# Kernel optimization log

Measured on AMD Instinct MI355X. Metric: run time of the kernel, lower is better.

## Reference

```python
import jax, jax.numpy as jnp
import numpy as np

B, N, M, H, W = 8, 8192, 4096, 128, 128


def setup_inputs() -> dict:
    key = jax.random.key(0)
    k1, k2, k3, k4 = jax.random.split(key, 4)
    xc_off_grid = jax.random.uniform(k1, (B, N, 2), dtype=jnp.float32)
    yc_off_grid = jax.random.normal(k2, (B, N), dtype=jnp.float32)
    # regular grid coords: meshgrid of two sorted 1-D axes, stacked on last dim
    xs = jnp.linspace(0.0, 1.0, H, dtype=jnp.float32)
    ys = jnp.linspace(0.0, 1.0, W, dtype=jnp.float32)
    gx, gy = jnp.meshgrid(xs, ys, indexing='ij')  # [H,W]
    xc_on_grid = jnp.broadcast_to(jnp.stack([gx, gy], -1), (B, H, W, 2))
    yc_on_grid = jax.random.normal(k3, (B, H, W), dtype=jnp.float32)
    # targets slightly outside [0,1] so interpn fill_value path is exercised
    xt = jax.random.uniform(k4, (B, M, 2), minval=-0.05, maxval=1.05, dtype=jnp.float32)
    mix_prop_logit = jnp.asarray(0.0, dtype=jnp.float32)
    return {"xc_off_grid": xc_off_grid, "yc_off_grid": yc_off_grid,
            "xc_on_grid": xc_on_grid, "yc_on_grid": yc_on_grid,
            "xt": xt, "mix_prop_logit": mix_prop_logit}


def _bilinear(xs, ys, vals, pts, fill):
    # interpn((xs, ys), vals, pts, bounds_error=False, fill_value=fill)
    x, y = pts[:, 0], pts[:, 1]
    ix = jnp.clip(jnp.searchsorted(xs, x, side='right') - 1, 0, xs.shape[0] - 2)
    iy = jnp.clip(jnp.searchsorted(ys, y, side='right') - 1, 0, ys.shape[0] - 2)
    wx = (x - xs[ix]) / (xs[ix + 1] - xs[ix])
    wy = (y - ys[iy]) / (ys[iy + 1] - ys[iy])
    v00 = vals[ix, iy]
    v01 = vals[ix, iy + 1]
    v10 = vals[ix + 1, iy]
    v11 = vals[ix + 1, iy + 1]
    v = ((1 - wx) * (1 - wy) * v00 + (1 - wx) * wy * v01
         + wx * (1 - wy) * v10 + wx * wy * v11)
    oob = (x < xs[0]) | (x > xs[-1]) | (y < ys[0]) | (y > ys[-1])
    return jnp.where(oob, fill, v)


def _per_batch(xc_off, yc_off, xc_on, yc_on, pts):
    # scattered interpolation: nearest-neighbor gather (stands in for
    # scipy griddata's Delaunay-linear; same irregular-access pattern)
    d2 = jnp.sum((pts[:, None, :] - xc_off[None, :, :]) ** 2, axis=-1)  # [M,N]
    yt_off = yc_off[jnp.argmin(d2, axis=1)]  # [M]
    # regular-grid bilinear, fill with grid mean outside bounds
    yt_on = _bilinear(xc_on[:, 0, 0], xc_on[0, :, 1], yc_on, pts, yc_on.mean())
    return yt_off, yt_on


def reference(xc_off_grid, yc_off_grid, xc_on_grid, yc_on_grid, xt, mix_prop_logit):
    yt_off, yt_on = jax.vmap(_per_batch)(xc_off_grid, yc_off_grid,
                                         xc_on_grid, yc_on_grid, xt)
    mix = jax.nn.sigmoid(mix_prop_logit)
    return mix * yt_off + (1 - mix) * yt_on  # [B, M]
```

## Files before the change

### kernel.cpp

```cpp
#include <hip/hip_runtime.h>
#include <math.h>
#include <float.h>

#define BB 8
#define NN 8192
#define MM 4096
#define HH 128
#define WW 128

#define G    32
#define GG   (G * G)
#define CELL (1.0f / G)

#define WS_COUNTS_OFF 256
#define WS_STARTS_OFF 33024
#define WS_CELLS_OFF  65824
#define WS_NEEDED     (WS_CELLS_OFF + (size_t)BB * NN * 16)

__device__ __forceinline__ int clampi(int v, int lo, int hi) {
    return v < lo ? lo : (v > hi ? hi : v);
}

__global__ void mean_zero_kernel(const float* __restrict__ yc_on,
                                 float* __restrict__ means,
                                 int* __restrict__ counts) {
    int b = blockIdx.x;
    if (counts) {
        int* c = counts + b * GG;
        for (int i = threadIdx.x; i < GG; i += blockDim.x) c[i] = 0;
    }
    const float* p = yc_on + b * (HH * WW);
    float s = 0.f;
    for (int i = threadIdx.x; i < HH * WW; i += blockDim.x) s += p[i];
    for (int off = 32; off > 0; off >>= 1) s += __shfl_down(s, off, 64);
    __shared__ float partial[4];
    int wave = threadIdx.x >> 6;
    if ((threadIdx.x & 63) == 0) partial[wave] = s;
    __syncthreads();
    if (threadIdx.x == 0) {
        float t = 0.f;
        int nw = blockDim.x >> 6;
        for (int i = 0; i < nw; ++i) t += partial[i];
        means[b] = t * (1.0f / (HH * WW));
    }
}

__global__ __launch_bounds__(256)
void count_kernel(const float* __restrict__ xc_off,
                  int* __restrict__ counts) {
    const int i = blockIdx.x * blockDim.x + threadIdx.x;
#pragma unroll
    for (int k = 0; k < 2; ++k) {
        const int idx = i + k * 32768;
        const int b = idx >> 13;
        const float2 c = ((const float2*)xc_off)[idx];
        const int gx = clampi((int)(c.x * (float)G), 0, G - 1);
        const int gy = clampi((int)(c.y * (float)G), 0, G - 1);
        atomicAdd(&counts[b * GG + gx * G + gy], 1);
    }
}

__global__ __launch_bounds__(1024)
void scan_kernel(int* __restrict__ counts,
                 int* __restrict__ starts) {
    const int b = blockIdx.x, tid = threadIdx.x;
    __shared__ int wsum[16];
    const int orig = counts[b * GG + tid];
    int x = orig;
    const int lane = tid & 63, wid = tid >> 6;
    for (int off = 1; off < 64; off <<= 1) {
        int y = __shfl_up(x, off, 64);
        if (lane >= off) x += y;
    }
    if (lane == 63) wsum[wid] = x;
    __syncthreads();
    if (tid < 16) {
        int w = wsum[tid];
        for (int off = 1; off < 16; off <<= 1) {
            int y = __shfl_up(w, off, 16);
            if (tid >= off) w += y;
        }
        wsum[tid] = w;
    }
    __syncthreads();
    const int incl = x + (wid ? wsum[wid - 1] : 0);
    const int excl = incl - orig;
    starts[b * (GG + 1) + tid] = excl;
    if (tid == GG - 1) starts[b * (GG + 1) + GG] = incl;
    counts[b * GG + tid] = excl;
}

__global__ __launch_bounds__(256)
void scatter_kernel(const float* __restrict__ xc_off,
                    const float* __restrict__ yc_off,
                    int* __restrict__ cursors,
                    float4* __restrict__ cellData) {
    const int i = blockIdx.x * blockDim.x + threadIdx.x;
#pragma unroll
    for (int k = 0; k < 2; ++k) {
        const int idx = i + k * 32768;
        const int b = idx >> 13;
        const int n = idx & (NN - 1);
        const float2 c = ((const float2*)xc_off)[idx];
        const float v = yc_off[idx];
        const int gx = clampi((int)(c.x * (float)G), 0, G - 1);
        const int gy = clampi((int)(c.y * (float)G), 0, G - 1);
        const int pos = atomicAdd(&cursors[b * GG + gx * G + gy], 1);
        cellData[(size_t)b * NN + pos] = make_float4(c.x, c.y, v, __int_as_float(n));
    }
}

__device__ __forceinline__ float epilogue(const float* __restrict__ yc_on,
                                          const float* __restrict__ means,
                                          const float* __restrict__ logit_p,
                                          int b, float px, float py, float bv) {
    const float* __restrict__ vals = yc_on + (size_t)b * HH * WW;
    const float x = px, y = py;
    int ix = clampi((int)floorf(x * 127.0f), 0, 126);
    int iy = clampi((int)floorf(y * 127.0f), 0, 126);
    const float x0 = (float)ix * (1.0f / 127.0f);
    const float x1 = (float)(ix + 1) * (1.0f / 127.0f);
    const float y0 = (float)iy * (1.0f / 127.0f);
    const float y1 = (float)(iy + 1) * (1.0f / 127.0f);
    const float wx = (x - x0) / (x1 - x0);
    const float wy = (y - y0) / (y1 - y0);
    const float v00 = vals[ix * WW + iy];
    const float v01 = vals[ix * WW + iy + 1];
    const float v10 = vals[(ix + 1) * WW + iy];
    const float v11 = vals[(ix + 1) * WW + iy + 1];
    float vi = (1.f - wx) * (1.f - wy) * v00
             + (1.f - wx) * wy         * v01
             + wx         * (1.f - wy) * v10
             + wx         * wy         * v11;
    const bool oob = (x < 0.f) || (x > 1.f) || (y < 0.f) || (y > 1.f);
    const float yon = oob ? means[b] : vi;
    const float l   = logit_p[0];
    const float mix = 1.f / (1.f + expf(-l));
    return mix * bv + (1.f - mix) * yon;
}

__global__ __launch_bounds__(256)
void query_kernel(const int* __restrict__ starts,
                  const float4* __restrict__ cellData,
                  const float* __restrict__ yc_on,
                  const float* __restrict__ xt,
                  const float* __restrict__ means,
                  const float* __restrict__ logit_p,
                  float* __restrict__ out)
{
    const int lane = threadIdx.x & 63;
    int pid = blockIdx.x * 4 + (threadIdx.x >> 6);
    pid = __builtin_amdgcn_readfirstlane(pid);
    const int b = pid >> 12;
    const int m = pid & (MM - 1);

    const float2 pt = ((const float2*)xt)[pid];
    const float px = pt.x, py = pt.y;

    const int cx = clampi((int)(px * (float)G), 0, G - 1);
    const int cy = clampi((int)(py * (float)G), 0, G - 1);

    const int*    __restrict__ st = starts + b * (GG + 1);
    const float4* __restrict__ cd = cellData + (size_t)b * NN;

    float bd = FLT_MAX;
    float bv = 0.f;
    int   bi = 0x7fffffff;

    for (int r = 1; r <= G; ++r) {
        const int gx0 = clampi(cx - r, 0, G - 1);
        const int gx1 = clampi(cx + r, 0, G - 1);
        const int gy0 = clampi(cy - r, 0, G - 1);
        const int gy1 = clampi(cy + r, 0, G - 1);

        for (int gx = gx0; gx <= gx1; ++gx) {
            const int lo = st[gx * G + gy0];
            const int hi = st[gx * G + gy1 + 1];
            for (int j = lo + lane; j < hi; j += 64) {
                const float4 c = cd[j];
                const float dx = px - c.x;
                const float dy = py - c.y;
                const float d2 = fmaf(dx, dx, dy * dy);
                const int   ci = __float_as_int(c.w);
                if (d2 < bd || (d2 == bd && ci < bi)) { bd = d2; bv = c.z; bi = ci; }
            }
        }

        for (int off = 1; off < 64; off <<= 1) {
            const float od = __shfl_xor(bd, off, 64);
            const float ov = __shfl_xor(bv, off, 64);
            const int   oi = __shfl_xor(bi, off, 64);
            if (od < bd || (od == bd && oi < bi)) { bd = od; bv = ov; bi = oi; }
        }

        const float rr = (float)r * CELL;
        if (rr * rr > bd) break;
    }

    if (lane == 0)
        out[(size_t)b * MM + m] = epilogue(yc_on, means, logit_p, b, px, py, bv);
}

#define WAVES 8
#define PTS 64
#define SLICE (NN / WAVES)

__global__ __launch_bounds__(WAVES * 64)
void nn_kernel(const float* __restrict__ xc_off,
               const float* __restrict__ yc_off,
               const float* __restrict__ yc_on,
               const float* __restrict__ xt,
               const float* __restrict__ means,
               const float* __restrict__ logit_p,
               float* __restrict__ out)
{
    const int blocksPerBatch = MM / PTS;
    const int b     = blockIdx.x / blocksPerBatch;
    const int pbase = (blockIdx.x % blocksPerBatch) * PTS;
    const int wave  = threadIdx.x >> 6;
    const int lane  = threadIdx.x & 63;
    const int m     = pbase + lane;

    const float2 pt = ((const float2*)xt)[b * MM + m];
    const float px = pt.x, py = pt.y;

    const float2* __restrict__ cxy = ((const float2*)xc_off) + (size_t)b * NN;
    const float*  __restrict__ cv  = yc_off + (size_t)b * NN;

    float best = 3.4e38f, bestv = 0.f;
    const int j0 = wave * SLICE;
    for (int t = 0; t < SLICE; t += 8) {
#pragma unroll
        for (int u = 0; u < 8; ++u) {
            const int j = j0 + t + u;
            const float2 c = cxy[j];
            const float  v = cv[j];
            const float dx = px - c.x;
            const float dy = py - c.y;
            const float d2 = fmaf(dx, dx, dy * dy);
            const bool lt = d2 < best;
            best  = lt ? d2 : best;
            bestv = lt ? v  : bestv;
        }
    }

    __shared__ float sd2[WAVES][PTS];
    __shared__ float sv [WAVES][PTS];
    sd2[wave][lane] = best;
    sv [wave][lane] = bestv;
    __syncthreads();

    if (threadIdx.x < PTS) {
        float bd = sd2[0][lane];
        float bv = sv [0][lane];
#pragma unroll
        for (int wv = 1; wv < WAVES; ++wv) {
            if (sd2[wv][lane] < bd) { bd = sd2[wv][lane]; bv = sv[wv][lane]; }
        }
        out[(size_t)b * MM + m] = epilogue(yc_on, means, logit_p, b, px, py, bv);
    }
}

extern "C" void kernel_launch(void* const* d_in, const int* in_sizes, int n_in,
                              void* d_out, int out_size, void* d_ws, size_t ws_size,
                              hipStream_t stream) {
    const float* xc_off = (const float*)d_in[0];
    const float* yc_off = (const float*)d_in[1];
    const float* yc_on  = (const float*)d_in[3];
    const float* xt     = (const float*)d_in[4];
    const float* logit  = (const float*)d_in[5];
    float* out = (float*)d_out;

    float* means = (float*)d_ws;

    if (ws_size >= WS_NEEDED) {
        int*    counts   = (int*)((char*)d_ws + WS_COUNTS_OFF);
        int*    starts   = (int*)((char*)d_ws + WS_STARTS_OFF);
        float4* cellData = (float4*)((char*)d_ws + WS_CELLS_OFF);

        mean_zero_kernel<<<BB, 256, 0, stream>>>(yc_on, means, counts);
        count_kernel<<<128, 256, 0, stream>>>(xc_off, counts);
        scan_kernel<<<BB, 1024, 0, stream>>>(counts, starts);
        scatter_kernel<<<128, 256, 0, stream>>>(xc_off, yc_off, counts, cellData);
        query_kernel<<<(BB * MM) / 4, 256, 0, stream>>>(
            starts, cellData, yc_on, xt, means, logit, out);
    } else {
        mean_zero_kernel<<<BB, 256, 0, stream>>>(yc_on, means, nullptr);
        nn_kernel<<<BB * (MM / PTS), WAVES * 64, 0, stream>>>(
            xc_off, yc_off, yc_on, xt, means, logit, out);
    }
}
```

Before: 113.4 us.

## Use half-wave per query, fold mean into scan, memset counts, widen grids

The query kernel now assigns 32 lanes per query point, so each 64-wide wave handles two queries and the cross-lane reduction is cut to five steps. The grid-mean reduction moves into the scan kernel, and the counts buffer is zeroed with hipMemsetAsync instead of a separate kernel. Count and scatter kernels launch one thread per point across more blocks instead of two points per thread. The aim is less lane idling in the sparse per-cell loops and fewer tiny launches. The cost is divergence between the two queries sharing a wave, since their search radii can differ.

```diff
diff --git a/kernel.cpp b/kernel.cpp
--- a/kernel.cpp
+++ b/kernel.cpp
@@ -21,50 +21,26 @@
     return v < lo ? lo : (v > hi ? hi : v);
 }
 
-__global__ void mean_zero_kernel(const float* __restrict__ yc_on,
-                                 float* __restrict__ means,
-                                 int* __restrict__ counts) {
-    int b = blockIdx.x;
-    if (counts) {
-        int* c = counts + b * GG;
-        for (int i = threadIdx.x; i < GG; i += blockDim.x) c[i] = 0;
-    }
-    const float* p = yc_on + b * (HH * WW);
-    float s = 0.f;
-    for (int i = threadIdx.x; i < HH * WW; i += blockDim.x) s += p[i];
-    for (int off = 32; off > 0; off >>= 1) s += __shfl_down(s, off, 64);
-    __shared__ float partial[4];
-    int wave = threadIdx.x >> 6;
-    if ((threadIdx.x & 63) == 0) partial[wave] = s;
-    __syncthreads();
-    if (threadIdx.x == 0) {
-        float t = 0.f;
-        int nw = blockDim.x >> 6;
-        for (int i = 0; i < nw; ++i) t += partial[i];
-        means[b] = t * (1.0f / (HH * WW));
-    }
-}
-
 __global__ __launch_bounds__(256)
 void count_kernel(const float* __restrict__ xc_off,
                   int* __restrict__ counts) {
-    const int i = blockIdx.x * blockDim.x + threadIdx.x;
-#pragma unroll
-    for (int k = 0; k < 2; ++k) {
-        const int idx = i + k * 32768;
-        const int b = idx >> 13;
-        const float2 c = ((const float2*)xc_off)[idx];
-        const int gx = clampi((int)(c.x * (float)G), 0, G - 1);
-        const int gy = clampi((int)(c.y * (float)G), 0, G - 1);
-        atomicAdd(&counts[b * GG + gx * G + gy], 1);
-    }
+    const int idx = blockIdx.x * blockDim.x + threadIdx.x;
+    const int b = idx >> 13;
+    const float2 c = ((const float2*)xc_off)[idx];
+    const int gx = clampi((int)(c.x * (float)G), 0, G - 1);
+    const int gy = clampi((int)(c.y * (float)G), 0, G - 1);
+    atomicAdd(&counts[b * GG + gx * G + gy], 1);
 }
 
 __global__ __launch_bounds__(1024)
-void scan_kernel(int* __restrict__ counts,
-                 int* __restrict__ starts) {
+void scan_mean_kernel(int* __restrict__ counts,
+                      int* __restrict__ starts,
+                      const float* __restrict__ yc_on,
+                      float* __restrict__ means) {
     const int b = blockIdx.x, tid = threadIdx.x;
-    __shared__ int wsum[16];
+    __shared__ int   wsum[16];
+    __shared__ float partial[4];
+
     const int orig = counts[b * GG + tid];
     int x = orig;
     const int lane = tid & 63, wid = tid >> 6;
@@ -88,6 +64,20 @@
     starts[b * (GG + 1) + tid] = excl;
     if (tid == GG - 1) starts[b * (GG + 1) + GG] = incl;
     counts[b * GG + tid] = excl;
+
+    float s = 0.f;
+    if (tid < 256) {
+        const float* p = yc_on + b * (HH * WW);
+        for (int i = tid; i < HH * WW; i += 256) s += p[i];
+        for (int off = 32; off > 0; off >>= 1) s += __shfl_down(s, off, 64);
+    }
+    if (tid < 256 && (tid & 63) == 0) partial[tid >> 6] = s;
+    __syncthreads();
+    if (tid == 0) {
+        float t = 0.f;
+        for (int i = 0; i < 4; ++i) t += partial[i];
+        means[b] = t * (1.0f / (HH * WW));
+    }
 }
 
 __global__ __launch_bounds__(256)
@@ -95,19 +85,15 @@
                     const float* __restrict__ yc_off,
                     int* __restrict__ cursors,
                     float4* __restrict__ cellData) {
-    const int i = blockIdx.x * blockDim.x + threadIdx.x;
-#pragma unroll
-    for (int k = 0; k < 2; ++k) {
-        const int idx = i + k * 32768;
-        const int b = idx >> 13;
-        const int n = idx & (NN - 1);
-        const float2 c = ((const float2*)xc_off)[idx];
-        const float v = yc_off[idx];
-        const int gx = clampi((int)(c.x * (float)G), 0, G - 1);
-        const int gy = clampi((int)(c.y * (float)G), 0, G - 1);
-        const int pos = atomicAdd(&cursors[b * GG + gx * G + gy], 1);
-        cellData[(size_t)b * NN + pos] = make_float4(c.x, c.y, v, __int_as_float(n));
-    }
+    const int idx = blockIdx.x * blockDim.x + threadIdx.x;
+    const int b = idx >> 13;
+    const int n = idx & (NN - 1);
+    const float2 c = ((const float2*)xc_off)[idx];
+    const float v = yc_off[idx];
+    const int gx = clampi((int)(c.x * (float)G), 0, G - 1);
+    const int gy = clampi((int)(c.y * (float)G), 0, G - 1);
+    const int pos = atomicAdd(&cursors[b * GG + gx * G + gy], 1);
+    cellData[(size_t)b * NN + pos] = make_float4(c.x, c.y, v, __int_as_float(n));
 }
 
 __device__ __forceinline__ float epilogue(const float* __restrict__ yc_on,
@@ -148,9 +134,8 @@
                   const float* __restrict__ logit_p,
                   float* __restrict__ out)
 {
-    const int lane = threadIdx.x & 63;
-    int pid = blockIdx.x * 4 + (threadIdx.x >> 6);
-    pid = __builtin_amdgcn_readfirstlane(pid);
+    const int lane32 = threadIdx.x & 31;
+    const int pid = blockIdx.x * 8 + (threadIdx.x >> 5);
     const int b = pid >> 12;
     const int m = pid & (MM - 1);
 
@@ -176,7 +161,7 @@
         for (int gx = gx0; gx <= gx1; ++gx) {
             const int lo = st[gx * G + gy0];
             const int hi = st[gx * G + gy1 + 1];
-            for (int j = lo + lane; j < hi; j += 64) {
+            for (int j = lo + lane32; j < hi; j += 32) {
                 const float4 c = cd[j];
                 const float dx = px - c.x;
                 const float dy = py - c.y;
@@ -186,7 +171,7 @@
             }
         }
 
-        for (int off = 1; off < 64; off <<= 1) {
+        for (int off = 1; off < 32; off <<= 1) {
             const float od = __shfl_xor(bd, off, 64);
             const float ov = __shfl_xor(bv, off, 64);
             const int   oi = __shfl_xor(bi, off, 64);
@@ -197,13 +182,32 @@
         if (rr * rr > bd) break;
     }
 
-    if (lane == 0)
+    if (lane32 == 0)
         out[(size_t)b * MM + m] = epilogue(yc_on, means, logit_p, b, px, py, bv);
 }
 
 #define WAVES 8
 #define PTS 64
 #define SLICE (NN / WAVES)
+
+__global__ void mean_kernel(const float* __restrict__ yc_on,
+                            float* __restrict__ means) {
+    int b = blockIdx.x;
+    const float* p = yc_on + b * (HH * WW);
+    float s = 0.f;
+    for (int i = threadIdx.x; i < HH * WW; i += blockDim.x) s += p[i];
+    for (int off = 32; off > 0; off >>= 1) s += __shfl_down(s, off, 64);
+    __shared__ float partial[4];
+    int wave = threadIdx.x >> 6;
+    if ((threadIdx.x & 63) == 0) partial[wave] = s;
+    __syncthreads();
+    if (threadIdx.x == 0) {
+        float t = 0.f;
+        int nw = blockDim.x >> 6;
+        for (int i = 0; i < nw; ++i) t += partial[i];
+        means[b] = t * (1.0f / (HH * WW));
+    }
+}
 
 __global__ __launch_bounds__(WAVES * 64)
 void nn_kernel(const float* __restrict__ xc_off,
@@ -278,14 +282,15 @@
         int*    starts   = (int*)((char*)d_ws + WS_STARTS_OFF);
         float4* cellData = (float4*)((char*)d_ws + WS_CELLS_OFF);
 
-        mean_zero_kernel<<<BB, 256, 0, stream>>>(yc_on, means, counts);
-        count_kernel<<<128, 256, 0, stream>>>(xc_off, counts);
-        scan_kernel<<<BB, 1024, 0, stream>>>(counts, starts);
-        scatter_kernel<<<128, 256, 0, stream>>>(xc_off, yc_off, counts, cellData);
-        query_kernel<<<(BB * MM) / 4, 256, 0, stream>>>(
+        hipMemsetAsync(counts, 0, (size_t)BB * GG * sizeof(int), stream);
+        count_kernel<<<(BB * NN) / 256, 256, 0, stream>>>(xc_off, counts);
+        scan_mean_kernel<<<BB, 1024, 0, stream>>>(counts, starts, yc_on, means);
+        scatter_kernel<<<(BB * NN) / 256, 256, 0, stream>>>(
+            xc_off, yc_off, counts, cellData);
+        query_kernel<<<(BB * MM) / 8, 256, 0, stream>>>(
             starts, cellData, yc_on, xt, means, logit, out);
     } else {
-        mean_zero_kernel<<<BB, 256, 0, stream>>>(yc_on, means, nullptr);
+        mean_kernel<<<BB, 256, 0, stream>>>(yc_on, means);
         nn_kernel<<<BB * (MM / PTS), WAVES * 64, 0, stream>>>(
             xc_off, yc_off, yc_on, xt, means, logit, out);
     }
```

Measured after the change: 105.9 us. -6.7%, faster.
